# Optimization experiments

Hardware: AMD Instinct MI355X
Metric: run time of the kernel (lower is better)

## Reference

```python
import jax, jax.numpy as jnp
import numpy as np

N_USERS = 10000
N_ITEMS = 100000
N_FEATURES = 64
EMB_DIM = 128
TAU = 0.01
NUM_SEQ = 100000
SEQ_LEN = 50


def setup_inputs() -> dict:
    key = jax.random.key(0)
    k1, k2, k3, k4, k5, k6 = jax.random.split(key, 6)
    users = jax.random.randint(k1, (NUM_SEQ,), 0, N_USERS, dtype=jnp.int32)
    items = jax.random.randint(k2, (NUM_SEQ,), 0, N_ITEMS, dtype=jnp.int32)
    R_ui = jax.random.normal(k3, (NUM_SEQ, SEQ_LEN, N_FEATURES), dtype=jnp.float32)
    mask = jax.random.randint(k4, (NUM_SEQ, SEQ_LEN), 0, 2).astype(bool)
    mask = mask.at[:, 0].set(True)  # ensure every sequence has >=1 valid step
    w = jax.random.normal(k5, (N_FEATURES,), dtype=jnp.float32)  # nn.init.normal_
    item_emb = jax.random.normal(k6, (N_ITEMS + 1, EMB_DIM), dtype=jnp.float32) * 0.1
    item_emb = item_emb.at[0].set(0.0)  # padding_idx=0
    alpha = jnp.ones((1,), jnp.float32)
    beta = jnp.ones((1,), jnp.float32)
    gamma = jnp.ones((1,), jnp.float32)
    return {"users": users, "items": items, "R_ui": R_ui, "mask": mask,
            "w": w, "item_emb": item_emb, "alpha": alpha, "beta": beta, "gamma": gamma}


def reference(users, items, R_ui, mask, w, item_emb, alpha, beta, gamma):
    # Z: [num_seq, seq_len] masked power-mean features
    Z = jnp.einsum('nsd,d->ns', R_ui, w)
    Wv = jnp.maximum(Z, TAU)                       # nn.Threshold(tau, tau)
    Wp = jnp.where(mask, Wv ** alpha, 0.0)         # W[~mask] = 0, then **alpha
    W_alpha = jnp.sum(Wp, axis=-1) ** (1.0 / alpha)
    R_beta = jnp.sum(mask, axis=-1).astype(R_ui.dtype) ** beta
    wt = (W_alpha * R_beta) ** gamma               # [num_seq]
    q = item_emb[items]                            # [num_seq, emb_dim]
    # per-user weighted average (replaces Python loop over users.unique())
    num = jax.ops.segment_sum(wt[:, None] * q, users, num_segments=N_USERS + 1)
    den = jax.ops.segment_sum(wt, users, num_segments=N_USERS + 1)
    p = num[users] / den[users][:, None]
    r = jnp.sum(p * q, axis=-1)                    # [num_seq]
    return r
```

## Files before the change

### kernel.cpp

```cpp
#include <hip/hip_runtime.h>
#include <hip/hip_bf16.h>
#include <stdint.h>

#define N_USERS   10000
#define N_ITEMS   100000
#define N_FEAT    64
#define EMB_DIM   128
#define SEQ_LEN   50
#define TAU       0.01f

typedef float f32x4 __attribute__((ext_vector_type(4)));

__device__ inline f32x4 nt_load4(const float* p) {
    return __builtin_nontemporal_load(reinterpret_cast<const f32x4*>(p));
}

__global__ __launch_bounds__(256) void wt_scatter_kernel(
    const float* __restrict__ R, const void* __restrict__ mask_raw,
    const float* __restrict__ w,
    const int* __restrict__ users, const int* __restrict__ items,
    const float* __restrict__ item_emb,
    const float* __restrict__ alpha_p, const float* __restrict__ beta_p,
    const float* __restrict__ gamma_p,
    float* __restrict__ num, float* __restrict__ den, int num_seq)
{
    int wave = (blockIdx.x * blockDim.x + threadIdx.x) >> 6;
    int lane = threadIdx.x & 63;
    if (wave >= num_seq) return;
    const int n = wave;

    const int u  = users[n];
    const int it = items[n];

    const unsigned int* mi = (const unsigned int*)mask_raw;
    unsigned int pv = mi[lane];
    float        pf = __uint_as_float(pv);
    bool allint = __all(pv <= 1u) != 0;
    bool allflt = __all(pf == 0.0f || pf == 1.0f) != 0;
    const int mode = allint ? 0 : (allflt ? 1 : 2);

    bool mv = false;
    if (lane < SEQ_LEN) {
        size_t off = (size_t)n * SEQ_LEN + lane;
        if (mode == 0)      mv = ((const int*)mask_raw)[off] != 0;
        else if (mode == 1) mv = ((const float*)mask_raw)[off] != 0.0f;
        else                mv = ((const uint8_t*)mask_raw)[off] != 0;
    }
    unsigned long long mbits = __ballot(mv);

    const float alpha = alpha_p[0];
    const float beta  = beta_p[0];
    const float gamma = gamma_p[0];

    const int f4 = lane & 15;
    const int sg = lane >> 4;

    const f32x4 w4 = *reinterpret_cast<const f32x4*>(w + 4 * f4);
    const float* Rn = R + (size_t)n * SEQ_LEN * N_FEAT;

    float acc = 0.0f;
    float cnt = 0.0f;

    #pragma unroll
    for (int s0 = 0; s0 < SEQ_LEN; s0 += 4) {
        int s = s0 + sg;
        bool valid = (s < SEQ_LEN);
        f32x4 x = {0.f, 0.f, 0.f, 0.f};
        if (valid) x = nt_load4(Rn + s * N_FEAT + 4 * f4);
        float d = x.x * w4.x + x.y * w4.y + x.z * w4.z + x.w * w4.w;
        d += __shfl_xor(d, 1);
        d += __shfl_xor(d, 2);
        d += __shfl_xor(d, 4);
        d += __shfl_xor(d, 8);
        if (valid && ((mbits >> s) & 1ULL)) {
            float Wv = fmaxf(d, TAU);
            acc += (alpha == 1.0f) ? Wv : powf(Wv, alpha);
            cnt += 1.0f;
        }
    }
    acc += __shfl_xor(acc, 16);
    acc += __shfl_xor(acc, 32);
    cnt += __shfl_xor(cnt, 16);
    cnt += __shfl_xor(cnt, 32);

    float W_alpha = (alpha == 1.0f) ? acc : powf(acc, 1.0f / alpha);
    float R_beta  = (beta  == 1.0f) ? cnt : powf(cnt, beta);
    float base    = W_alpha * R_beta;
    float wt      = (gamma == 1.0f) ? base : powf(base, gamma);

    const float2 q = reinterpret_cast<const float2*>(item_emb + (size_t)it * EMB_DIM)[lane];
    float* numrow = num + (size_t)u * EMB_DIM;
    atomicAdd(&numrow[2 * lane],     wt * q.x);
    atomicAdd(&numrow[2 * lane + 1], wt * q.y);
    if (lane == 0) atomicAdd(&den[u], wt);
}

__global__ __launch_bounds__(256) void final_kernel(
    const int* __restrict__ users, const int* __restrict__ items,
    const float* __restrict__ item_emb,
    const float* __restrict__ num, const float* __restrict__ den,
    float* __restrict__ r, int num_seq)
{
    int wave = (blockIdx.x * blockDim.x + threadIdx.x) >> 6;
    int lane = threadIdx.x & 63;
    if (wave >= num_seq) return;
    const int n = wave;

    int u  = users[n];
    int it = items[n];
    float2 q = reinterpret_cast<const float2*>(item_emb + (size_t)it * EMB_DIM)[lane];
    float2 p = reinterpret_cast<const float2*>(num + (size_t)u * EMB_DIM)[lane];
    float dot = q.x * p.x + q.y * p.y;
    dot += __shfl_xor(dot, 1);
    dot += __shfl_xor(dot, 2);
    dot += __shfl_xor(dot, 4);
    dot += __shfl_xor(dot, 8);
    dot += __shfl_xor(dot, 16);
    dot += __shfl_xor(dot, 32);
    if (lane == 0) r[n] = dot / den[u];
}

extern "C" void kernel_launch(void* const* d_in, const int* in_sizes, int n_in,
                              void* d_out, int out_size, void* d_ws, size_t ws_size,
                              hipStream_t stream)
{
    const int*   users    = (const int*)d_in[0];
    const int*   items    = (const int*)d_in[1];
    const float* R_ui     = (const float*)d_in[2];
    const void*  mask     = d_in[3];
    const float* w        = (const float*)d_in[4];
    const float* item_emb = (const float*)d_in[5];
    const float* alpha    = (const float*)d_in[6];
    const float* beta     = (const float*)d_in[7];
    const float* gamma    = (const float*)d_in[8];

    const int num_seq = in_sizes[0];
    float* num = (float*)d_ws;
    float* den = (float*)d_ws + (size_t)N_USERS * EMB_DIM;

    (void)hipMemsetAsync(d_ws, 0,
                         ((size_t)N_USERS * EMB_DIM + N_USERS) * sizeof(float),
                         stream);

    {
        int waves_per_block = 4;
        int blocks = (num_seq + waves_per_block - 1) / waves_per_block;
        wt_scatter_kernel<<<blocks, 256, 0, stream>>>(R_ui, mask, w, users, items,
                                                      item_emb, alpha, beta, gamma,
                                                      num, den, num_seq);
    }
    {
        int waves_per_block = 4;
        int blocks = (num_seq + waves_per_block - 1) / waves_per_block;
        final_kernel<<<blocks, 256, 0, stream>>>(users, items, item_emb,
                                                 num, den, (float*)d_out, num_seq);
    }
}
```

Before: 272.9 us.

## Fuse scatter and final passes into one cooperative persistent kernel with grid sync

Merges the weighted-scatter kernel and the final dot-product kernel into a single cooperative kernel. It uses grid-stride persistent waves and a grid.sync() between the two phases. Per-wave setup (mask mode detection, w load, parameter reads) is hoisted out of the per-sequence loop. This removes one kernel launch and amortizes setup, at the cost of a grid-wide barrier and reduced occupancy from the capped grid size. It falls back to the two-kernel path if the cooperative launch fails.

```diff
diff --git a/kernel.cpp b/kernel.cpp
--- a/kernel.cpp
+++ b/kernel.cpp
@@ -1,6 +1,9 @@
 #include <hip/hip_runtime.h>
 #include <hip/hip_bf16.h>
+#include <hip/hip_cooperative_groups.h>
 #include <stdint.h>
+
+namespace cg = cooperative_groups;
 
 #define N_USERS   10000
 #define N_ITEMS   100000
@@ -8,6 +11,7 @@
 #define EMB_DIM   128
 #define SEQ_LEN   50
 #define TAU       0.01f
+#define N_CU      256
 
 typedef float f32x4 __attribute__((ext_vector_type(4)));
 
@@ -15,30 +19,19 @@
     return __builtin_nontemporal_load(reinterpret_cast<const f32x4*>(p));
 }
 
-__global__ __launch_bounds__(256) void wt_scatter_kernel(
-    const float* __restrict__ R, const void* __restrict__ mask_raw,
-    const float* __restrict__ w,
-    const int* __restrict__ users, const int* __restrict__ items,
-    const float* __restrict__ item_emb,
-    const float* __restrict__ alpha_p, const float* __restrict__ beta_p,
-    const float* __restrict__ gamma_p,
-    float* __restrict__ num, float* __restrict__ den, int num_seq)
-{
-    int wave = (blockIdx.x * blockDim.x + threadIdx.x) >> 6;
-    int lane = threadIdx.x & 63;
-    if (wave >= num_seq) return;
-    const int n = wave;
-
-    const int u  = users[n];
-    const int it = items[n];
-
+
+__device__ inline int detect_mask_mode(const void* mask_raw, int lane) {
     const unsigned int* mi = (const unsigned int*)mask_raw;
     unsigned int pv = mi[lane];
     float        pf = __uint_as_float(pv);
     bool allint = __all(pv <= 1u) != 0;
     bool allflt = __all(pf == 0.0f || pf == 1.0f) != 0;
-    const int mode = allint ? 0 : (allflt ? 1 : 2);
-
+    return allint ? 0 : (allflt ? 1 : 2);
+}
+
+__device__ inline unsigned long long load_mask_ballot(
+    const void* mask_raw, int mode, int n, int lane)
+{
     bool mv = false;
     if (lane < SEQ_LEN) {
         size_t off = (size_t)n * SEQ_LEN + lane;
@@ -46,16 +39,19 @@
         else if (mode == 1) mv = ((const float*)mask_raw)[off] != 0.0f;
         else                mv = ((const uint8_t*)mask_raw)[off] != 0;
     }
-    unsigned long long mbits = __ballot(mv);
-
-    const float alpha = alpha_p[0];
-    const float beta  = beta_p[0];
-    const float gamma = gamma_p[0];
-
-    const int f4 = lane & 15;
-    const int sg = lane >> 4;
-
-    const f32x4 w4 = *reinterpret_cast<const f32x4*>(w + 4 * f4);
+    return __ballot(mv);
+}
+
+__device__ inline void wt_scatter_seq(
+    int n, int lane, int f4, int sg, f32x4 w4,
+    const float* __restrict__ R, unsigned long long mbits,
+    float alpha, float beta, float gamma,
+    const int* __restrict__ users, const int* __restrict__ items,
+    const float* __restrict__ item_emb,
+    float* __restrict__ num, float* __restrict__ den)
+{
+    const int u  = users[n];
+    const int it = items[n];
     const float* Rn = R + (size_t)n * SEQ_LEN * N_FEAT;
 
     float acc = 0.0f;
@@ -95,17 +91,13 @@
     if (lane == 0) atomicAdd(&den[u], wt);
 }
 
-__global__ __launch_bounds__(256) void final_kernel(
+__device__ inline void final_seq(
+    int n, int lane,
     const int* __restrict__ users, const int* __restrict__ items,
     const float* __restrict__ item_emb,
     const float* __restrict__ num, const float* __restrict__ den,
-    float* __restrict__ r, int num_seq)
-{
-    int wave = (blockIdx.x * blockDim.x + threadIdx.x) >> 6;
-    int lane = threadIdx.x & 63;
-    if (wave >= num_seq) return;
-    const int n = wave;
-
+    float* __restrict__ r)
+{
     int u  = users[n];
     int it = items[n];
     float2 q = reinterpret_cast<const float2*>(item_emb + (size_t)it * EMB_DIM)[lane];
@@ -120,6 +112,88 @@
     if (lane == 0) r[n] = dot / den[u];
 }
 
+__global__ __launch_bounds__(256, 4) void fused_kernel(
+    const float* __restrict__ R, const void* __restrict__ mask_raw,
+    const float* __restrict__ w,
+    const int* __restrict__ users, const int* __restrict__ items,
+    const float* __restrict__ item_emb,
+    const float* __restrict__ alpha_p, const float* __restrict__ beta_p,
+    const float* __restrict__ gamma_p,
+    float* __restrict__ num, float* __restrict__ den,
+    float* __restrict__ r, int num_seq)
+{
+    cg::grid_group grid = cg::this_grid();
+
+    const int lane   = threadIdx.x & 63;
+    const int wib    = threadIdx.x >> 6;
+    const int wpb    = blockDim.x >> 6;
+    const int gwave  = blockIdx.x * wpb + wib;
+    const int nwaves = gridDim.x * wpb;
+
+    const int mode = detect_mask_mode(mask_raw, lane);
+
+    const float alpha = alpha_p[0];
+    const float beta  = beta_p[0];
+    const float gamma = gamma_p[0];
+
+    const int f4 = lane & 15;
+    const int sg = lane >> 4;
+    const f32x4 w4 = *reinterpret_cast<const f32x4*>(w + 4 * f4);
+
+    for (int n = gwave; n < num_seq; n += nwaves) {
+        unsigned long long mbits = load_mask_ballot(mask_raw, mode, n, lane);
+        wt_scatter_seq(n, lane, f4, sg, w4, R, mbits, alpha, beta, gamma,
+                       users, items, item_emb, num, den);
+    }
+
+    grid.sync();
+
+    for (int n = gwave; n < num_seq; n += nwaves) {
+        final_seq(n, lane, users, items, item_emb, num, den, r);
+    }
+}
+
+__global__ __launch_bounds__(256) void wt_scatter_kernel(
+    const float* __restrict__ R, const void* __restrict__ mask_raw,
+    const float* __restrict__ w,
+    const int* __restrict__ users, const int* __restrict__ items,
+    const float* __restrict__ item_emb,
+    const float* __restrict__ alpha_p, const float* __restrict__ beta_p,
+    const float* __restrict__ gamma_p,
+    float* __restrict__ num, float* __restrict__ den, int num_seq)
+{
+    int wave = (blockIdx.x * blockDim.x + threadIdx.x) >> 6;
+    int lane = threadIdx.x & 63;
+    if (wave >= num_seq) return;
+    const int n = wave;
+
+    const int mode = detect_mask_mode(mask_raw, lane);
+    unsigned long long mbits = load_mask_ballot(mask_raw, mode, n, lane);
+
+    const float alpha = alpha_p[0];
+    const float beta  = beta_p[0];
+    const float gamma = gamma_p[0];
+
+    const int f4 = lane & 15;
+    const int sg = lane >> 4;
+    const f32x4 w4 = *reinterpret_cast<const f32x4*>(w + 4 * f4);
+
+    wt_scatter_seq(n, lane, f4, sg, w4, R, mbits, alpha, beta, gamma,
+                   users, items, item_emb, num, den);
+}
+
+__global__ __launch_bounds__(256) void final_kernel(
+    const int* __restrict__ users, const int* __restrict__ items,
+    const float* __restrict__ item_emb,
+    const float* __restrict__ num, const float* __restrict__ den,
+    float* __restrict__ r, int num_seq)
+{
+    int wave = (blockIdx.x * blockDim.x + threadIdx.x) >> 6;
+    int lane = threadIdx.x & 63;
+    if (wave >= num_seq) return;
+    final_seq(wave, lane, users, items, item_emb, num, den, r);
+}
+
 extern "C" void kernel_launch(void* const* d_in, const int* in_sizes, int n_in,
                               void* d_out, int out_size, void* d_ws, size_t ws_size,
                               hipStream_t stream)
@@ -134,25 +208,39 @@
     const float* beta     = (const float*)d_in[7];
     const float* gamma    = (const float*)d_in[8];
 
-    const int num_seq = in_sizes[0];
+    int num_seq = in_sizes[0];
     float* num = (float*)d_ws;
     float* den = (float*)d_ws + (size_t)N_USERS * EMB_DIM;
+    float* rout = (float*)d_out;
 
     (void)hipMemsetAsync(d_ws, 0,
                          ((size_t)N_USERS * EMB_DIM + N_USERS) * sizeof(float),
                          stream);
 
-    {
+    hipError_t cerr = hipErrorUnknown;
+    int maxBlocksPerCU = 0;
+    hipError_t qerr = hipOccupancyMaxActiveBlocksPerMultiprocessor(
+        &maxBlocksPerCU, fused_kernel, 256, 0);
+    if (qerr == hipSuccess && maxBlocksPerCU > 0) {
+        int grid = maxBlocksPerCU * N_CU;
+        if (grid > 2048) grid = 2048;
+        void* args[] = {
+            (void*)&R_ui, (void*)&mask, (void*)&w,
+            (void*)&users, (void*)&items, (void*)&item_emb,
+            (void*)&alpha, (void*)&beta, (void*)&gamma,
+            (void*)&num, (void*)&den, (void*)&rout, (void*)&num_seq,
+        };
+        cerr = hipLaunchCooperativeKernel((const void*)fused_kernel,
+                                          dim3(grid), dim3(256), args, 0, stream);
+    }
+
+    if (cerr != hipSuccess) {
         int waves_per_block = 4;
         int blocks = (num_seq + waves_per_block - 1) / waves_per_block;
         wt_scatter_kernel<<<blocks, 256, 0, stream>>>(R_ui, mask, w, users, items,
                                                       item_emb, alpha, beta, gamma,
                                                       num, den, num_seq);
-    }
-    {
-        int waves_per_block = 4;
-        int blocks = (num_seq + waves_per_block - 1) / waves_per_block;
         final_kernel<<<blocks, 256, 0, stream>>>(users, items, item_emb,
-                                                 num, den, (float*)d_out, num_seq);
-    }
-}
+                                                 num, den, rout, num_seq);
+    }
+}
```

Result: slower. 481.4 us (+76.4%).
